# Kernel tuning notes

Hardware: AMD Instinct MI355X
Metric: run time of the kernel (lower is better)

Reference implementation:

```python
import jax, jax.numpy as jnp
import numpy as np


def setup_inputs() -> dict:
    key = jax.random.key(0)
    ks = jax.random.split(key, 9)
    B, D_IN, UNITS, TOPICS, VOCAB = 64, 512, 1024, 20, 32000
    return {
        "inputs": jax.random.normal(ks[0], (B, D_IN), jnp.float32),
        "prev_state": jax.random.normal(ks[1], (B, UNITS), jnp.float32),
        "kernel": jax.random.normal(ks[2], (D_IN, UNITS), jnp.float32) * 0.02,
        "recurrent_kernel": jax.random.normal(ks[3], (UNITS, UNITS), jnp.float32) * 0.02,
        "bernoli_kernel": jax.random.normal(ks[4], (UNITS, 1), jnp.float32) * 0.02,
        "vocab_kernel": jax.random.normal(ks[5], (UNITS, VOCAB), jnp.float32) * 0.02,
        "beta": jax.random.normal(ks[6], (TOPICS, VOCAB), jnp.float32),
        "indicators": jax.random.randint(ks[7], (B,), 0, 2, jnp.int32),
        "indices": jax.random.randint(ks[8], (B,), 0, VOCAB, jnp.int32),
    }


def reference(inputs, prev_state, kernel, recurrent_kernel, bernoli_kernel,
              vocab_kernel, beta, indicators, indices):
    # h_t = x @ W_xh + h_{t-1} @ W_hh   -> [B, units]
    next_state = inputs @ kernel + prev_state @ recurrent_kernel
    # stop-word Bernoulli prob: sigmoid(softplus(h_t @ w_b))  -> [B, 1]
    bern_p = jax.nn.sigmoid(jax.nn.softplus(next_state @ bernoli_kernel))
    bern_p = bern_p[..., None]  # [B, 1, 1]
    # deterministic sampling key (reference baseline)
    samp_key = jax.random.key(42)
    bern_samples = jax.random.bernoulli(samp_key, bern_p).astype(jnp.float32)
    # logits: [B,1,V] + (1 - l_t) * beta[T,V] -> [B, T, V]
    logits = (next_state @ vocab_kernel)[:, None, :] + (1.0 - bern_samples) * beta
    word_prob_out = jax.nn.softmax(logits, axis=-1)
    return word_prob_out, next_state
```

## Files before the change

### kernel.cpp

```cpp
#include <hip/hip_runtime.h>
#include <cstdint>
#include <cstddef>

typedef unsigned int u32;
typedef unsigned short u16;

#define NB 64
#define DIN 512
#define UNITS 1024
#define TOPICS 20
#define VOCAB 32000
#define NS_OFF ((size_t)NB * TOPICS * VOCAB)
#define ESV_PART ((size_t)NB * VOCAB)

typedef __attribute__((ext_vector_type(8))) short s16x8;
typedef __attribute__((ext_vector_type(4))) float f32x4;

__device__ __forceinline__ float bf2f(u16 h) {
    union { u32 u; float f; } c; c.u = ((u32)h) << 16; return c.f;
}
__device__ __forceinline__ u16 f2bf(float f) {
    union { float f; u32 u; } c; c.f = f;
    u32 r = c.u + 0x7FFFu + ((c.u >> 16) & 1u);
    return (u16)(r >> 16);
}
template<bool F32>
__device__ __forceinline__ float ldv(const void* p, size_t i) {
    if constexpr (F32) return ((const float*)p)[i];
    else return bf2f(((const u16*)p)[i]);
}
__device__ __forceinline__ float ldr(const void* p, size_t i, bool f32) {
    return f32 ? ((const float*)p)[i] : bf2f(((const u16*)p)[i]);
}

__device__ __forceinline__ u32 threefry_bits_partitionable(u32 i) {
    const u32 ks0 = 0u, ks1 = 42u, ks2 = 0u ^ 42u ^ 0x1BD11BDAu;
    u32 x0 = 0u + ks0, x1 = i + ks1;
#define TF_R(r) { x0 += x1; x1 = (x1 << r) | (x1 >> (32 - r)); x1 ^= x0; }
    TF_R(13) TF_R(15) TF_R(26) TF_R(6)
    x0 += ks1; x1 += ks2 + 1u;
    TF_R(17) TF_R(29) TF_R(16) TF_R(24)
    x0 += ks2; x1 += ks0 + 2u;
    TF_R(13) TF_R(15) TF_R(26) TF_R(6)
    x0 += ks0; x1 += ks1 + 3u;
    TF_R(17) TF_R(29) TF_R(16) TF_R(24)
    x0 += ks1; x1 += ks2 + 4u;
    TF_R(13) TF_R(15) TF_R(26) TF_R(6)
    x0 += ks2; x1 += ks0 + 5u;
#undef TF_R
    return x0 ^ x1;
}

__global__ __launch_bounds__(256)
void k_init(const void* __restrict__ beta, int* __restrict__ flag,
            float* __restrict__ lsum, float* __restrict__ eb) {
    int tid = threadIdx.x, lane = tid & 63, w = tid >> 6;
    __shared__ int cnt_s[4];
    int cnt = 0;
    const u32* braw = (const u32*)beta;
    for (int i = tid; i < 1024; i += 256) {
        u32 x = braw[i];
        u32 e = (x >> 7) & 0xFFu;
        cnt += (e >= 110u && e <= 132u) ? 1 : 0;
    }
    for (int off = 32; off; off >>= 1) cnt += __shfl_down(cnt, off, 64);
    if (lane == 0) cnt_s[w] = cnt;
    __syncthreads();
    int total = cnt_s[0] + cnt_s[1] + cnt_s[2] + cnt_s[3];
    bool f32 = total < 512;

    size_t base = (size_t)blockIdx.x * 2000;
    for (int i = tid; i < 2000; i += 256)
        eb[base + i] = __expf(ldr(beta, base + i, f32));

    if (blockIdx.x == 0) {
        for (int i = tid; i < NB * TOPICS; i += 256) lsum[i] = 0.f;
        if (tid == 0) flag[0] = f32 ? 1 : 0;
    }
}

template<bool F32>
__device__ void state_body(const void* xin, const void* h0, const void* Wxh,
                           const void* Whh, float* ns_f32, void* dout) {
    __shared__ float lx[DIN + UNITS];
    int b = blockIdx.x >> 2;
    int u = ((blockIdx.x & 3) << 8) | threadIdx.x;
    for (int i = threadIdx.x; i < DIN; i += 256)
        lx[i] = ldv<F32>(xin, (size_t)b * DIN + i);
    for (int i = threadIdx.x; i < UNITS; i += 256)
        lx[DIN + i] = ldv<F32>(h0, (size_t)b * UNITS + i);
    __syncthreads();
    float acc = 0.f;
#pragma unroll 8
    for (int k = 0; k < DIN; ++k)   acc += lx[k]       * ldv<F32>(Wxh, (size_t)k * UNITS + u);
#pragma unroll 8
    for (int k = 0; k < UNITS; ++k) acc += lx[DIN + k] * ldv<F32>(Whh, (size_t)k * UNITS + u);
    int idx = b * UNITS + u;
    ns_f32[idx] = acc;
    if constexpr (F32) ((float*)dout)[NS_OFF + idx] = acc;
    else               ((u16*)dout)[NS_OFF + idx]   = f2bf(acc);
}
__global__ __launch_bounds__(256)
void k_state(const int* __restrict__ flag, const void* xin, const void* h0,
             const void* Wxh, const void* Whh,
             float* __restrict__ ns_f32, void* dout) {
    if (*flag) state_body<true>(xin, h0, Wxh, Whh, ns_f32, dout);
    else       state_body<false>(xin, h0, Wxh, Whh, ns_f32, dout);
}

template<bool F32>
__device__ void bern_body(const float* ns, const void* bk, float* coeff) {
    int b = blockIdx.x, lane = threadIdx.x;
    float s = 0.f;
#pragma unroll
    for (int i = 0; i < UNITS / 64; ++i) {
        int k = lane + (i << 6);
        s += ns[b * UNITS + k] * ldv<F32>(bk, k);
    }
    for (int off = 32; off; off >>= 1) s += __shfl_down(s, off, 64);
    if (lane == 0) {
        float sp = log1pf(expf(s));
        float p  = 1.f / (1.f + expf(-sp));
        u32 bits = threefry_bits_partitionable((u32)b);
        union { u32 u; float f; } c; c.u = (bits >> 9) | 0x3f800000u;
        float uni = c.f - 1.0f;
        coeff[b] = (uni < p) ? 0.f : 1.f;
    }
}
__global__ __launch_bounds__(64)
void k_bern(const int* __restrict__ flag, const float* __restrict__ ns,
            const void* bk, float* __restrict__ coeff) {
    if (*flag) bern_body<true>(ns, bk, coeff);
    else       bern_body<false>(ns, bk, coeff);
}

#define PAD 68
#define SV_BB 16384
#define SV_SMEM_BYTES 34816

__device__ void sv_mfma_body(const short* __restrict__ ns16,
                             const short* __restrict__ Wv,
                             float* __restrict__ esv4, char* smem, int pos) {
    const int tid  = threadIdx.x;
    const int lane = tid & 63;
    const int wn   = tid >> 6;
    const int g    = lane >> 4;
    const int l15  = lane & 15;

    const int vb = pos % 125, kb = pos / 125;
    const int v0 = vb * 256;
    const int kbase0 = kb * 256;

    const int w5 = tid >> 5, c31 = tid & 31;
    const short* bs0 = Wv + (size_t)(kbase0 +  0 + w5) * VOCAB + v0 + ((c31 ^ 0) << 3);
    const short* bs1 = Wv + (size_t)(kbase0 +  8 + w5) * VOCAB + v0 + ((c31 ^ 1) << 3);
    const short* bs2 = Wv + (size_t)(kbase0 + 16 + w5) * VOCAB + v0 + ((c31 ^ 2) << 3);
    const short* bs3 = Wv + (size_t)(kbase0 + 24 + w5) * VOCAB + v0 + ((c31 ^ 3) << 3);
    const short* as0 = ns16 + (size_t)(l15     ) * UNITS + kbase0 + g * 8;
    const short* as1 = ns16 + (size_t)(l15 + 16) * UNITS + kbase0 + g * 8;
    const short* as2 = ns16 + (size_t)(l15 + 32) * UNITS + kbase0 + g * 8;
    const short* as3 = ns16 + (size_t)(l15 + 48) * UNITS + kbase0 + g * 8;

    float4 bE0, bE1, bE2, bE3;
    float4 bO0, bO1, bO2, bO3;
    s16x8  aE0, aE1, aE2, aE3;
    s16x8  aO0, aO1, aO2, aO3;

    f32x4 acc[4][4];
#pragma unroll
    for (int m = 0; m < 4; ++m)
#pragma unroll
        for (int n = 0; n < 4; ++n) acc[m][n] = (f32x4){0.f, 0.f, 0.f, 0.f};

#define LOADB(T, R0, R1, R2, R3) {                                        \
    size_t ko = (size_t)(T) * 32 * VOCAB;                                 \
    R0 = *(const float4*)(bs0 + ko); R1 = *(const float4*)(bs1 + ko);     \
    R2 = *(const float4*)(bs2 + ko); R3 = *(const float4*)(bs3 + ko); }
#define LOADA(T, A0, A1, A2, A3) {                                        \
    int ko = (T) * 32;                                                    \
    A0 = *(const s16x8*)(as0 + ko); A1 = *(const s16x8*)(as1 + ko);       \
    A2 = *(const s16x8*)(as2 + ko); A3 = *(const s16x8*)(as3 + ko); }
#define WRITEB(BUF, R0, R1, R2, R3) {                                     \
    float4* d = (float4*)(smem + (BUF) * SV_BB);                          \
    d[tid] = R0; d[256 + tid] = R1; d[512 + tid] = R2; d[768 + tid] = R3; }
#define COMPUTE(BUF, A0, A1, A2, A3) {                                    \
    const short* Bs = (const short*)(smem + (BUF) * SV_BB);               \
    _Pragma("unroll")                                                     \
    for (int nf = 0; nf < 4; ++nf) {                                      \
        int col = wn * 64 + nf * 16 + l15;                                \
        int b0  = (((col >> 3) ^ g) << 3) + (col & 7);                    \
        s16x8 bf;                                                         \
        _Pragma("unroll")                                                 \
        for (int e = 0; e < 8; ++e) bf[e] = Bs[(g * 8 + e) * 256 + b0];   \
        acc[0][nf] = __builtin_amdgcn_mfma_f32_16x16x32_bf16(A0, bf, acc[0][nf], 0, 0, 0); \
        acc[1][nf] = __builtin_amdgcn_mfma_f32_16x16x32_bf16(A1, bf, acc[1][nf], 0, 0, 0); \
        acc[2][nf] = __builtin_amdgcn_mfma_f32_16x16x32_bf16(A2, bf, acc[2][nf], 0, 0, 0); \
        acc[3][nf] = __builtin_amdgcn_mfma_f32_16x16x32_bf16(A3, bf, acc[3][nf], 0, 0, 0); } }
#define VMW(N)  asm volatile("s_waitcnt vmcnt(" #N ")" ::: "memory");
#define LGK0    asm volatile("s_waitcnt lgkmcnt(0)" ::: "memory");
#define BAR     __builtin_amdgcn_s_barrier();

    LOADB(0, bE0, bE1, bE2, bE3)
    LOADA(0, aE0, aE1, aE2, aE3)
    LOADB(1, bO0, bO1, bO2, bO3)
    VMW(8)
    WRITEB(0, bE0, bE1, bE2, bE3)
    LGK0

    LOADB(2, bE0, bE1, bE2, bE3)  LOADA(1, aO0, aO1, aO2, aO3)
    BAR  VMW(8)  WRITEB(1, bO0, bO1, bO2, bO3)  LGK0
    COMPUTE(0, aE0, aE1, aE2, aE3)
    LOADB(3, bO0, bO1, bO2, bO3)  LOADA(2, aE0, aE1, aE2, aE3)
    BAR  VMW(8)  WRITEB(0, bE0, bE1, bE2, bE3)  LGK0
    COMPUTE(1, aO0, aO1, aO2, aO3)
    LOADB(4, bE0, bE1, bE2, bE3)  LOADA(3, aO0, aO1, aO2, aO3)
    BAR  VMW(8)  WRITEB(1, bO0, bO1, bO2, bO3)  LGK0
    COMPUTE(2, aE0, aE1, aE2, aE3)
    LOADB(5, bO0, bO1, bO2, bO3)  LOADA(4, aE0, aE1, aE2, aE3)
    BAR  VMW(8)  WRITEB(0, bE0, bE1, bE2, bE3)  LGK0
    COMPUTE(3, aO0, aO1, aO2, aO3)
    LOADB(6, bE0, bE1, bE2, bE3)  LOADA(5, aO0, aO1, aO2, aO3)
    BAR  VMW(8)  WRITEB(1, bO0, bO1, bO2, bO3)  LGK0
    COMPUTE(4, aE0, aE1, aE2, aE3)
    LOADB(7, bO0, bO1, bO2, bO3)  LOADA(6, aE0, aE1, aE2, aE3)
    BAR  VMW(8)  WRITEB(0, bE0, bE1, bE2, bE3)  LGK0
    COMPUTE(5, aO0, aO1, aO2, aO3)
    LOADA(7, aO0, aO1, aO2, aO3)
    BAR  VMW(4)  WRITEB(1, bO0, bO1, bO2, bO3)  LGK0
    COMPUTE(6, aE0, aE1, aE2, aE3)
    BAR  VMW(0)
    COMPUTE(7, aO0, aO1, aO2, aO3)

#undef LOADB
#undef LOADA
#undef WRITEB
#undef COMPUTE
#undef VMW
#undef LGK0
#undef BAR

    float* dst = esv4 + (size_t)kb * ESV_PART + v0;
#pragma unroll
    for (int mf = 0; mf < 4; ++mf)
#pragma unroll
        for (int nf = 0; nf < 4; ++nf) {
            int col = wn * 64 + nf * 16 + l15;
#pragma unroll
            for (int r = 0; r < 4; ++r) {
                int b = mf * 16 + (lane >> 4) * 4 + r;
                dst[(size_t)b * VOCAB + col] = acc[mf][nf][r];
            }
        }
}

__device__ void sv_f32_body(const float* __restrict__ ns, const float* __restrict__ Wv,
                            float* __restrict__ esv4, float* As, float* Bs, int pos) {
    int tid = threadIdx.x;
    int vt = tid & 7;
    int bg = tid >> 3;
    int v0 = pos * 64;
    float acc[2][8];
#pragma unroll
    for (int r = 0; r < 2; ++r)
#pragma unroll
        for (int j = 0; j < 8; ++j) acc[r][j] = 0.f;

    for (int k0 = 0; k0 < UNITS; k0 += 64) {
        __syncthreads();
        for (int e = tid; e < 1024; e += 256) {
            int row = e >> 4, c4 = e & 15;
            *(float4*)&As[row * PAD + c4 * 4] =
                *(const float4*)&ns[row * UNITS + k0 + c4 * 4];
        }
        for (int e = tid; e < 1024; e += 256) {
            int row = e >> 4, c4 = e & 15;
            *(float4*)&Bs[row * PAD + c4 * 4] =
                *(const float4*)(Wv + (size_t)(k0 + row) * VOCAB + v0 + c4 * 4);
        }
        __syncthreads();
#pragma unroll 4
        for (int u = 0; u < 64; u += 4) {
            float4 a0 = *(float4*)&As[(bg * 2 + 0) * PAD + u];
            float4 a1 = *(float4*)&As[(bg * 2 + 1) * PAD + u];
            float aa0[4] = {a0.x, a0.y, a0.z, a0.w};
            float aa1[4] = {a1.x, a1.y, a1.z, a1.w};
#pragma unroll
            for (int uu = 0; uu < 4; ++uu) {
                float4 b0 = *(float4*)&Bs[(u + uu) * PAD + vt * 8];
                float4 b1 = *(float4*)&Bs[(u + uu) * PAD + vt * 8 + 4];
                float bb[8] = {b0.x, b0.y, b0.z, b0.w, b1.x, b1.y, b1.z, b1.w};
#pragma unroll
                for (int j = 0; j < 8; ++j) {
                    acc[0][j] = fmaf(aa0[uu], bb[j], acc[0][j]);
                    acc[1][j] = fmaf(aa1[uu], bb[j], acc[1][j]);
                }
            }
        }
    }
#pragma unroll
    for (int r = 0; r < 2; ++r) {
        float4 e0 = {acc[r][0], acc[r][1], acc[r][2], acc[r][3]};
        float4 e1 = {acc[r][4], acc[r][5], acc[r][6], acc[r][7]};
        float* dst = esv4 + (size_t)(bg * 2 + r) * VOCAB + v0 + vt * 8;
        *(float4*)dst = e0;
        *(float4*)(dst + 4) = e1;
    }
}

__global__ __launch_bounds__(256, 3)
void k_sv(const int* __restrict__ flag, const float* __restrict__ ns,
          const void* Wv, const void* dout, float* __restrict__ esv4) {
    __shared__ __align__(16) char smem[SV_SMEM_BYTES];
    int lin = blockIdx.x;
    int xcd = lin & 7, idx = lin >> 3;
    int pos = (xcd < 4) ? xcd * 63 + idx : 252 + (xcd - 4) * 62 + idx;
    if (*flag) {
        float* As = (float*)smem;
        sv_f32_body(ns, (const float*)Wv, esv4, As, As + 64 * PAD, pos);
    } else {
        sv_mfma_body((const short*)dout + NS_OFF, (const short*)Wv, esv4, smem, pos);
    }
}

__global__ __launch_bounds__(256)
void k_sum(const int* __restrict__ flag, const float* __restrict__ esv4,
           const float* __restrict__ eb, const float* __restrict__ coeff,
           float* __restrict__ lsum) {
    int b = blockIdx.y, tid = threadIdx.x;
    bool f32 = (*flag != 0);
    float c = coeff[b];
    const float4* P0 = (const float4*)(esv4 + (size_t)b * VOCAB);
    const float4* P1 = (const float4*)(esv4 + ESV_PART + (size_t)b * VOCAB);
    const float4* P2 = (const float4*)(esv4 + 2 * ESV_PART + (size_t)b * VOCAB);
    const float4* P3 = (const float4*)(esv4 + 3 * ESV_PART + (size_t)b * VOCAB);
    int i0 = blockIdx.x * 256 + tid;
    __shared__ float red[4][TOPICS];
    int lane = tid & 63, w = tid >> 6;

    if (c != 0.f) {
        float acc[TOPICS];
#pragma unroll
        for (int t = 0; t < TOPICS; ++t) acc[t] = 0.f;
        for (int i = i0; i < VOCAB / 4; i += 4096) {
            float4 q = P0[i];
            if (!f32) {
                float4 a = P1[i], d = P2[i], h = P3[i];
                q.x += a.x + d.x + h.x; q.y += a.y + d.y + h.y;
                q.z += a.z + d.z + h.z; q.w += a.w + d.w + h.w;
            }
            float4 e;
            e.x = __expf(q.x); e.y = __expf(q.y);
            e.z = __expf(q.z); e.w = __expf(q.w);
#pragma unroll
            for (int t = 0; t < TOPICS; ++t) {
                float4 g = *(const float4*)(eb + (size_t)t * VOCAB + i * 4);
                acc[t] += e.x * g.x + e.y * g.y + e.z * g.z + e.w * g.w;
            }
        }
#pragma unroll
        for (int t = 0; t < TOPICS; ++t) {
            float v = acc[t];
            for (int off = 32; off; off >>= 1) v += __shfl_down(v, off, 64);
            if (lane == 0) red[w][t] = v;
        }
        __syncthreads();
        if (tid < TOPICS) {
            float s = red[0][tid] + red[1][tid] + red[2][tid] + red[3][tid];
            atomicAdd(&lsum[b * TOPICS + tid], s);
        }
    } else {
        float a = 0.f;
        for (int i = i0; i < VOCAB / 4; i += 4096) {
            float4 q = P0[i];
            if (!f32) {
                float4 x = P1[i], d = P2[i], h = P3[i];
                q.x += x.x + d.x + h.x; q.y += x.y + d.y + h.y;
                q.z += x.z + d.z + h.z; q.w += x.w + d.w + h.w;
            }
            a += __expf(q.x) + __expf(q.y) + __expf(q.z) + __expf(q.w);
        }
        for (int off = 32; off; off >>= 1) a += __shfl_down(a, off, 64);
        if (lane == 0) red[w][0] = a;
        __syncthreads();
        if (tid < TOPICS) {
            float s = red[0][0] + red[1][0] + red[2][0] + red[3][0];
            atomicAdd(&lsum[b * TOPICS + tid], s);
        }
    }
}

template<bool F32>
__device__ void write_body(const float* esv4, const float* eb, const float* coeff,
                           const float* lsum, void* dout) {
    int b = blockIdx.y, tid = threadIdx.x;
    int v0 = blockIdx.x * 2048 + tid * 8;
    if (v0 >= VOCAB) return;
    float c = coeff[b];
    const float* er = esv4 + (size_t)b * VOCAB + v0;
    float4 q0 = *(const float4*)er;
    float4 q1 = *(const float4*)(er + 4);
    if constexpr (!F32) {
#pragma unroll
        for (int p = 1; p < 4; ++p) {
            float4 a0 = *(const float4*)(er + p * ESV_PART);
            float4 a1 = *(const float4*)(er + p * ESV_PART + 4);
            q0.x += a0.x; q0.y += a0.y; q0.z += a0.z; q0.w += a0.w;
            q1.x += a1.x; q1.y += a1.y; q1.z += a1.z; q1.w += a1.w;
        }
    }
    float4 e0, e1;
    e0.x = __expf(q0.x); e0.y = __expf(q0.y); e0.z = __expf(q0.z); e0.w = __expf(q0.w);
    e1.x = __expf(q1.x); e1.y = __expf(q1.y); e1.z = __expf(q1.z); e1.w = __expf(q1.w);
#pragma unroll 4
    for (int t = 0; t < TOPICS; ++t) {
        float inv = 1.0f / lsum[b * TOPICS + t];
        float o0, o1, o2, o3, o4, o5, o6, o7;
        if (c != 0.f) {
            const float* gr = eb + (size_t)t * VOCAB + v0;
            float4 g0 = *(const float4*)gr;
            float4 g1 = *(const float4*)(gr + 4);
            o0 = e0.x * g0.x * inv; o1 = e0.y * g0.y * inv;
            o2 = e0.z * g0.z * inv; o3 = e0.w * g0.w * inv;
            o4 = e1.x * g1.x * inv; o5 = e1.y * g1.y * inv;
            o6 = e1.z * g1.z * inv; o7 = e1.w * g1.w * inv;
        } else {
            o0 = e0.x * inv; o1 = e0.y * inv; o2 = e0.z * inv; o3 = e0.w * inv;
            o4 = e1.x * inv; o5 = e1.y * inv; o6 = e1.z * inv; o7 = e1.w * inv;
        }
        size_t off = (size_t)b * TOPICS * VOCAB + (size_t)t * VOCAB + v0;
        if constexpr (F32) {
            float4 s0 = {o0, o1, o2, o3}, s1 = {o4, o5, o6, o7};
            *(float4*)((float*)dout + off) = s0;
            *(float4*)((float*)dout + off + 4) = s1;
        } else {
            uint4 st;
            st.x = (u32)f2bf(o0) | ((u32)f2bf(o1) << 16);
            st.y = (u32)f2bf(o2) | ((u32)f2bf(o3) << 16);
            st.z = (u32)f2bf(o4) | ((u32)f2bf(o5) << 16);
            st.w = (u32)f2bf(o6) | ((u32)f2bf(o7) << 16);
            *(uint4*)((u16*)dout + off) = st;
        }
    }
}
__global__ __launch_bounds__(256)
void k_write(const int* __restrict__ flag, const float* __restrict__ esv4,
             const float* __restrict__ eb, const float* __restrict__ coeff,
             const float* __restrict__ lsum, void* dout) {
    if (*flag) write_body<true>(esv4, eb, coeff, lsum, dout);
    else       write_body<false>(esv4, eb, coeff, lsum, dout);
}

extern "C" void kernel_launch(void* const* d_in, const int* in_sizes, int n_in,
                              void* d_out, int out_size, void* d_ws, size_t ws_size,
                              hipStream_t stream) {
    const void* xin  = d_in[0];
    const void* h0   = d_in[1];
    const void* Wxh  = d_in[2];
    const void* Whh  = d_in[3];
    const void* bk   = d_in[4];
    const void* Wv   = d_in[5];
    const void* beta = d_in[6];

    char* ws = (char*)d_ws;
    int*   flag   = (int*)  (ws + 0);
    float* coeff  = (float*)(ws + 256);
    float* lsum   = (float*)(ws + 1024);
    float* ns_f32 = (float*)(ws + 8192);
    float* eb     = (float*)(ws + 270336);
    float* esv4   = (float*)(ws + 2830336);

    k_init <<<320, 256, 0, stream>>>(beta, flag, lsum, eb);
    k_state<<<256, 256, 0, stream>>>(flag, xin, h0, Wxh, Whh, ns_f32, d_out);
    k_bern <<<64, 64, 0, stream>>>(flag, ns_f32, bk, coeff);
    k_sv   <<<500, 256, 0, stream>>>(flag, ns_f32, Wv, d_out, esv4);
    k_sum  <<<dim3(16, 64), 256, 0, stream>>>(flag, esv4, eb, coeff, lsum);
    k_write<<<dim3(16, 64), 256, 0, stream>>>(flag, esv4, eb, coeff, lsum, d_out);
}
```

Before: 483.7 us.

## Split state GEMM over K halves and split vocab GEMM into four K-launches

The recurrent-state GEMM is split into two K halves across twice as many blocks, and the partial sums are added in the Bernoulli kernel, which now also writes next_state to the output. The vocab GEMM tile is narrowed from 256 to 64 columns per block and issued as four separate launches, one per 256-wide K chunk, each writing its own partial-sum slab. The f32 path now also produces four partials, so the sum and write kernels always add them. The aim is more parallelism and less per-block register and shared-memory pressure, at the cost of extra launches, partial-sum traffic and less B-tile reuse per block.

```diff
diff --git a/kernel.cpp b/kernel.cpp
--- a/kernel.cpp
+++ b/kernel.cpp
@@ -81,41 +81,52 @@
 
 template<bool F32>
 __device__ void state_body(const void* xin, const void* h0, const void* Wxh,
-                           const void* Whh, float* ns_f32, void* dout) {
-    __shared__ float lx[DIN + UNITS];
-    int b = blockIdx.x >> 2;
-    int u = ((blockIdx.x & 3) << 8) | threadIdx.x;
-    for (int i = threadIdx.x; i < DIN; i += 256)
-        lx[i] = ldv<F32>(xin, (size_t)b * DIN + i);
-    for (int i = threadIdx.x; i < UNITS; i += 256)
-        lx[DIN + i] = ldv<F32>(h0, (size_t)b * UNITS + i);
+                           const void* Whh, float* ns_p) {
+    __shared__ float lx[768];
+    int bid  = blockIdx.x;
+    int b    = bid >> 3;
+    int uq   = (bid >> 1) & 3;
+    int half = bid & 1;
+    int u = (uq << 8) | threadIdx.x;
+    for (int i = threadIdx.x; i < 768; i += 256) {
+        int kk = half * 768 + i;
+        lx[i] = (kk < DIN) ? ldv<F32>(xin, (size_t)b * DIN + kk)
+                           : ldv<F32>(h0,  (size_t)b * UNITS + (kk - DIN));
+    }
     __syncthreads();
     float acc = 0.f;
+    if (half == 0) {
 #pragma unroll 8
-    for (int k = 0; k < DIN; ++k)   acc += lx[k]       * ldv<F32>(Wxh, (size_t)k * UNITS + u);
+        for (int k = 0; k < DIN; ++k) acc += lx[k] * ldv<F32>(Wxh, (size_t)k * UNITS + u);
 #pragma unroll 8
-    for (int k = 0; k < UNITS; ++k) acc += lx[DIN + k] * ldv<F32>(Whh, (size_t)k * UNITS + u);
-    int idx = b * UNITS + u;
-    ns_f32[idx] = acc;
-    if constexpr (F32) ((float*)dout)[NS_OFF + idx] = acc;
-    else               ((u16*)dout)[NS_OFF + idx]   = f2bf(acc);
+        for (int k = 0; k < 256; ++k) acc += lx[DIN + k] * ldv<F32>(Whh, (size_t)k * UNITS + u);
+    } else {
+#pragma unroll 8
+        for (int k = 0; k < 768; ++k) acc += lx[k] * ldv<F32>(Whh, (size_t)(256 + k) * UNITS + u);
+    }
+    ns_p[half * (NB * UNITS) + b * UNITS + u] = acc;
 }
 __global__ __launch_bounds__(256)
 void k_state(const int* __restrict__ flag, const void* xin, const void* h0,
-             const void* Wxh, const void* Whh,
-             float* __restrict__ ns_f32, void* dout) {
-    if (*flag) state_body<true>(xin, h0, Wxh, Whh, ns_f32, dout);
-    else       state_body<false>(xin, h0, Wxh, Whh, ns_f32, dout);
+             const void* Wxh, const void* Whh, float* __restrict__ ns_p) {
+    if (*flag) state_body<true>(xin, h0, Wxh, Whh, ns_p);
+    else       state_body<false>(xin, h0, Wxh, Whh, ns_p);
 }
 
 template<bool F32>
-__device__ void bern_body(const float* ns, const void* bk, float* coeff) {
+__device__ void bern_body(const float* ns_p, const void* bk, float* coeff,
+                          float* ns_f32, void* dout) {
     int b = blockIdx.x, lane = threadIdx.x;
     float s = 0.f;
 #pragma unroll
     for (int i = 0; i < UNITS / 64; ++i) {
         int k = lane + (i << 6);
-        s += ns[b * UNITS + k] * ldv<F32>(bk, k);
+        int idx = b * UNITS + k;
+        float v = ns_p[idx] + ns_p[NB * UNITS + idx];
+        ns_f32[idx] = v;
+        if constexpr (F32) ((float*)dout)[NS_OFF + idx] = v;
+        else               ((u16*)dout)[NS_OFF + idx]   = f2bf(v);
+        s += v * ldv<F32>(bk, k);
     }
     for (int off = 32; off; off >>= 1) s += __shfl_down(s, off, 64);
     if (lane == 0) {
@@ -128,105 +139,94 @@
     }
 }
 __global__ __launch_bounds__(64)
-void k_bern(const int* __restrict__ flag, const float* __restrict__ ns,
-            const void* bk, float* __restrict__ coeff) {
-    if (*flag) bern_body<true>(ns, bk, coeff);
-    else       bern_body<false>(ns, bk, coeff);
+void k_bern(const int* __restrict__ flag, const float* __restrict__ ns_p,
+            const void* bk, float* __restrict__ coeff,
+            float* __restrict__ ns_f32, void* dout) {
+    if (*flag) bern_body<true>(ns_p, bk, coeff, ns_f32, dout);
+    else       bern_body<false>(ns_p, bk, coeff, ns_f32, dout);
 }
 
 #define PAD 68
-#define SV_BB 16384
+#define SV_BB 4096
 #define SV_SMEM_BYTES 34816
 
 __device__ void sv_mfma_body(const short* __restrict__ ns16,
                              const short* __restrict__ Wv,
-                             float* __restrict__ esv4, char* smem, int pos) {
+                             float* __restrict__ esv4, char* smem,
+                             int pos, int kb) {
     const int tid  = threadIdx.x;
     const int lane = tid & 63;
     const int wn   = tid >> 6;
     const int g    = lane >> 4;
     const int l15  = lane & 15;
 
-    const int vb = pos % 125, kb = pos / 125;
-    const int v0 = vb * 256;
+    const int v0 = pos * 64;
     const int kbase0 = kb * 256;
 
-    const int w5 = tid >> 5, c31 = tid & 31;
-    const short* bs0 = Wv + (size_t)(kbase0 +  0 + w5) * VOCAB + v0 + ((c31 ^ 0) << 3);
-    const short* bs1 = Wv + (size_t)(kbase0 +  8 + w5) * VOCAB + v0 + ((c31 ^ 1) << 3);
-    const short* bs2 = Wv + (size_t)(kbase0 + 16 + w5) * VOCAB + v0 + ((c31 ^ 2) << 3);
-    const short* bs3 = Wv + (size_t)(kbase0 + 24 + w5) * VOCAB + v0 + ((c31 ^ 3) << 3);
+    const int bk_ = tid >> 3, bc_ = tid & 7;
+    const short* bsrc = Wv + (size_t)(kbase0 + bk_) * VOCAB + v0
+                      + ((bc_ ^ (bk_ >> 3)) << 3);
     const short* as0 = ns16 + (size_t)(l15     ) * UNITS + kbase0 + g * 8;
     const short* as1 = ns16 + (size_t)(l15 + 16) * UNITS + kbase0 + g * 8;
     const short* as2 = ns16 + (size_t)(l15 + 32) * UNITS + kbase0 + g * 8;
     const short* as3 = ns16 + (size_t)(l15 + 48) * UNITS + kbase0 + g * 8;
 
-    float4 bE0, bE1, bE2, bE3;
-    float4 bO0, bO1, bO2, bO3;
+    float4 bE, bO;
     s16x8  aE0, aE1, aE2, aE3;
     s16x8  aO0, aO1, aO2, aO3;
 
-    f32x4 acc[4][4];
-#pragma unroll
-    for (int m = 0; m < 4; ++m)
-#pragma unroll
-        for (int n = 0; n < 4; ++n) acc[m][n] = (f32x4){0.f, 0.f, 0.f, 0.f};
-
-#define LOADB(T, R0, R1, R2, R3) {                                        \
-    size_t ko = (size_t)(T) * 32 * VOCAB;                                 \
-    R0 = *(const float4*)(bs0 + ko); R1 = *(const float4*)(bs1 + ko);     \
-    R2 = *(const float4*)(bs2 + ko); R3 = *(const float4*)(bs3 + ko); }
+    f32x4 acc[4];
+#pragma unroll
+    for (int m = 0; m < 4; ++m) acc[m] = (f32x4){0.f, 0.f, 0.f, 0.f};
+
+#define LOADB(T, R)  { R = *(const float4*)(bsrc + (size_t)(T) * 32 * VOCAB); }
 #define LOADA(T, A0, A1, A2, A3) {                                        \
     int ko = (T) * 32;                                                    \
     A0 = *(const s16x8*)(as0 + ko); A1 = *(const s16x8*)(as1 + ko);       \
     A2 = *(const s16x8*)(as2 + ko); A3 = *(const s16x8*)(as3 + ko); }
-#define WRITEB(BUF, R0, R1, R2, R3) {                                     \
-    float4* d = (float4*)(smem + (BUF) * SV_BB);                          \
-    d[tid] = R0; d[256 + tid] = R1; d[512 + tid] = R2; d[768 + tid] = R3; }
+#define WRITEB(BUF, R)  { ((float4*)(smem + (BUF) * SV_BB))[tid] = R; }
 #define COMPUTE(BUF, A0, A1, A2, A3) {                                    \
     const short* Bs = (const short*)(smem + (BUF) * SV_BB);               \
+    int col = wn * 16 + l15;                                              \
+    int b0  = (((col >> 3) ^ g) << 3) + (col & 7);                        \
+    s16x8 bf;                                                             \
     _Pragma("unroll")                                                     \
-    for (int nf = 0; nf < 4; ++nf) {                                      \
-        int col = wn * 64 + nf * 16 + l15;                                \
-        int b0  = (((col >> 3) ^ g) << 3) + (col & 7);                    \
-        s16x8 bf;                                                         \
-        _Pragma("unroll")                                                 \
-        for (int e = 0; e < 8; ++e) bf[e] = Bs[(g * 8 + e) * 256 + b0];   \
-        acc[0][nf] = __builtin_amdgcn_mfma_f32_16x16x32_bf16(A0, bf, acc[0][nf], 0, 0, 0); \
-        acc[1][nf] = __builtin_amdgcn_mfma_f32_16x16x32_bf16(A1, bf, acc[1][nf], 0, 0, 0); \
-        acc[2][nf] = __builtin_amdgcn_mfma_f32_16x16x32_bf16(A2, bf, acc[2][nf], 0, 0, 0); \
-        acc[3][nf] = __builtin_amdgcn_mfma_f32_16x16x32_bf16(A3, bf, acc[3][nf], 0, 0, 0); } }
+    for (int e = 0; e < 8; ++e) bf[e] = Bs[(g * 8 + e) * 64 + b0];        \
+    acc[0] = __builtin_amdgcn_mfma_f32_16x16x32_bf16(A0, bf, acc[0], 0, 0, 0); \
+    acc[1] = __builtin_amdgcn_mfma_f32_16x16x32_bf16(A1, bf, acc[1], 0, 0, 0); \
+    acc[2] = __builtin_amdgcn_mfma_f32_16x16x32_bf16(A2, bf, acc[2], 0, 0, 0); \
+    acc[3] = __builtin_amdgcn_mfma_f32_16x16x32_bf16(A3, bf, acc[3], 0, 0, 0); }
 #define VMW(N)  asm volatile("s_waitcnt vmcnt(" #N ")" ::: "memory");
 #define LGK0    asm volatile("s_waitcnt lgkmcnt(0)" ::: "memory");
 #define BAR     __builtin_amdgcn_s_barrier();
 
-    LOADB(0, bE0, bE1, bE2, bE3)
+    LOADB(0, bE)
     LOADA(0, aE0, aE1, aE2, aE3)
-    LOADB(1, bO0, bO1, bO2, bO3)
-    VMW(8)
-    WRITEB(0, bE0, bE1, bE2, bE3)
+    LOADB(1, bO)
+    VMW(5)
+    WRITEB(0, bE)
     LGK0
 
-    LOADB(2, bE0, bE1, bE2, bE3)  LOADA(1, aO0, aO1, aO2, aO3)
-    BAR  VMW(8)  WRITEB(1, bO0, bO1, bO2, bO3)  LGK0
+    LOADB(2, bE)  LOADA(1, aO0, aO1, aO2, aO3)
+    BAR  VMW(5)  WRITEB(1, bO)  LGK0
     COMPUTE(0, aE0, aE1, aE2, aE3)
-    LOADB(3, bO0, bO1, bO2, bO3)  LOADA(2, aE0, aE1, aE2, aE3)
-    BAR  VMW(8)  WRITEB(0, bE0, bE1, bE2, bE3)  LGK0
+    LOADB(3, bO)  LOADA(2, aE0, aE1, aE2, aE3)
+    BAR  VMW(5)  WRITEB(0, bE)  LGK0
     COMPUTE(1, aO0, aO1, aO2, aO3)
-    LOADB(4, bE0, bE1, bE2, bE3)  LOADA(3, aO0, aO1, aO2, aO3)
-    BAR  VMW(8)  WRITEB(1, bO0, bO1, bO2, bO3)  LGK0
+    LOADB(4, bE)  LOADA(3, aO0, aO1, aO2, aO3)
+    BAR  VMW(5)  WRITEB(1, bO)  LGK0
     COMPUTE(2, aE0, aE1, aE2, aE3)
-    LOADB(5, bO0, bO1, bO2, bO3)  LOADA(4, aE0, aE1, aE2, aE3)
-    BAR  VMW(8)  WRITEB(0, bE0, bE1, bE2, bE3)  LGK0
+    LOADB(5, bO)  LOADA(4, aE0, aE1, aE2, aE3)
+    BAR  VMW(5)  WRITEB(0, bE)  LGK0
     COMPUTE(3, aO0, aO1, aO2, aO3)
-    LOADB(6, bE0, bE1, bE2, bE3)  LOADA(5, aO0, aO1, aO2, aO3)
-    BAR  VMW(8)  WRITEB(1, bO0, bO1, bO2, bO3)  LGK0
+    LOADB(6, bE)  LOADA(5, aO0, aO1, aO2, aO3)
+    BAR  VMW(5)  WRITEB(1, bO)  LGK0
     COMPUTE(4, aE0, aE1, aE2, aE3)
-    LOADB(7, bO0, bO1, bO2, bO3)  LOADA(6, aE0, aE1, aE2, aE3)
-    BAR  VMW(8)  WRITEB(0, bE0, bE1, bE2, bE3)  LGK0
+    LOADB(7, bO)  LOADA(6, aE0, aE1, aE2, aE3)
+    BAR  VMW(5)  WRITEB(0, bE)  LGK0
     COMPUTE(5, aO0, aO1, aO2, aO3)
     LOADA(7, aO0, aO1, aO2, aO3)
-    BAR  VMW(4)  WRITEB(1, bO0, bO1, bO2, bO3)  LGK0
+    BAR  VMW(4)  WRITEB(1, bO)  LGK0
     COMPUTE(6, aE0, aE1, aE2, aE3)
     BAR  VMW(0)
     COMPUTE(7, aO0, aO1, aO2, aO3)
@@ -240,21 +240,19 @@
 #undef BAR
 
     float* dst = esv4 + (size_t)kb * ESV_PART + v0;
+    const int col = wn * 16 + l15;
 #pragma unroll
     for (int mf = 0; mf < 4; ++mf)
 #pragma unroll
-        for (int nf = 0; nf < 4; ++nf) {
-            int col = wn * 64 + nf * 16 + l15;
-#pragma unroll
-            for (int r = 0; r < 4; ++r) {
-                int b = mf * 16 + (lane >> 4) * 4 + r;
-                dst[(size_t)b * VOCAB + col] = acc[mf][nf][r];
-            }
+        for (int r = 0; r < 4; ++r) {
+            int b = mf * 16 + (lane >> 4) * 4 + r;
+            dst[(size_t)b * VOCAB + col] = acc[mf][r];
         }
 }
 
 __device__ void sv_f32_body(const float* __restrict__ ns, const float* __restrict__ Wv,
-                            float* __restrict__ esv4, float* As, float* Bs, int pos) {
+                            float* __restrict__ esv4, float* As, float* Bs,
+                            int pos, int kb) {
     int tid = threadIdx.x;
     int vt = tid & 7;
     int bg = tid >> 3;
@@ -265,7 +263,7 @@
 #pragma unroll
         for (int j = 0; j < 8; ++j) acc[r][j] = 0.f;
 
-    for (int k0 = 0; k0 < UNITS; k0 += 64) {
+    for (int k0 = kb * 256; k0 < kb * 256 + 256; k0 += 64) {
         __syncthreads();
         for (int e = tid; e < 1024; e += 256) {
             int row = e >> 4, c4 = e & 15;
@@ -297,11 +295,12 @@
             }
         }
     }
+    float* base = esv4 + (size_t)kb * ESV_PART;
 #pragma unroll
     for (int r = 0; r < 2; ++r) {
         float4 e0 = {acc[r][0], acc[r][1], acc[r][2], acc[r][3]};
         float4 e1 = {acc[r][4], acc[r][5], acc[r][6], acc[r][7]};
-        float* dst = esv4 + (size_t)(bg * 2 + r) * VOCAB + v0 + vt * 8;
+        float* dst = base + (size_t)(bg * 2 + r) * VOCAB + v0 + vt * 8;
         *(float4*)dst = e0;
         *(float4*)(dst + 4) = e1;
     }
@@ -309,25 +308,24 @@
 
 __global__ __launch_bounds__(256, 3)
 void k_sv(const int* __restrict__ flag, const float* __restrict__ ns,
-          const void* Wv, const void* dout, float* __restrict__ esv4) {
+          const void* Wv, const void* dout, float* __restrict__ esv4, int kb) {
     __shared__ __align__(16) char smem[SV_SMEM_BYTES];
     int lin = blockIdx.x;
     int xcd = lin & 7, idx = lin >> 3;
     int pos = (xcd < 4) ? xcd * 63 + idx : 252 + (xcd - 4) * 62 + idx;
     if (*flag) {
         float* As = (float*)smem;
-        sv_f32_body(ns, (const float*)Wv, esv4, As, As + 64 * PAD, pos);
+        sv_f32_body(ns, (const float*)Wv, esv4, As, As + 64 * PAD, pos, kb);
     } else {
-        sv_mfma_body((const short*)dout + NS_OFF, (const short*)Wv, esv4, smem, pos);
+        sv_mfma_body((const short*)dout + NS_OFF, (const short*)Wv, esv4, smem,
+                     pos, kb);
     }
 }
 
 __global__ __launch_bounds__(256)
-void k_sum(const int* __restrict__ flag, const float* __restrict__ esv4,
-           const float* __restrict__ eb, const float* __restrict__ coeff,
-           float* __restrict__ lsum) {
+void k_sum(const float* __restrict__ esv4, const float* __restrict__ eb,
+           const float* __restrict__ coeff, float* __restrict__ lsum) {
     int b = blockIdx.y, tid = threadIdx.x;
-    bool f32 = (*flag != 0);
     float c = coeff[b];
     const float4* P0 = (const float4*)(esv4 + (size_t)b * VOCAB);
     const float4* P1 = (const float4*)(esv4 + ESV_PART + (size_t)b * VOCAB);
@@ -343,11 +341,9 @@
         for (int t = 0; t < TOPICS; ++t) acc[t] = 0.f;
         for (int i = i0; i < VOCAB / 4; i += 4096) {
             float4 q = P0[i];
-            if (!f32) {
-                float4 a = P1[i], d = P2[i], h = P3[i];
-                q.x += a.x + d.x + h.x; q.y += a.y + d.y + h.y;
-                q.z += a.z + d.z + h.z; q.w += a.w + d.w + h.w;
-            }
+            float4 a = P1[i], d = P2[i], h = P3[i];
+            q.x += a.x + d.x + h.x; q.y += a.y + d.y + h.y;
+            q.z += a.z + d.z + h.z; q.w += a.w + d.w + h.w;
             float4 e;
             e.x = __expf(q.x); e.y = __expf(q.y);
             e.z = __expf(q.z); e.w = __expf(q.w);
@@ -372,11 +368,9 @@
         float a = 0.f;
         for (int i = i0; i < VOCAB / 4; i += 4096) {
             float4 q = P0[i];
-            if (!f32) {
-                float4 x = P1[i], d = P2[i], h = P3[i];
-                q.x += x.x + d.x + h.x; q.y += x.y + d.y + h.y;
-                q.z += x.z + d.z + h.z; q.w += x.w + d.w + h.w;
-            }
+            float4 x = P1[i], d = P2[i], h = P3[i];
+            q.x += x.x + d.x + h.x; q.y += x.y + d.y + h.y;
+            q.z += x.z + d.z + h.z; q.w += x.w + d.w + h.w;
             a += __expf(q.x) + __expf(q.y) + __expf(q.z) + __expf(q.w);
         }
         for (int off = 32; off; off >>= 1) a += __shfl_down(a, off, 64);
@@ -399,14 +393,12 @@
     const float* er = esv4 + (size_t)b * VOCAB + v0;
     float4 q0 = *(const float4*)er;
     float4 q1 = *(const float4*)(er + 4);
-    if constexpr (!F32) {
-#pragma unroll
-        for (int p = 1; p < 4; ++p) {
-            float4 a0 = *(const float4*)(er + p * ESV_PART);
-            float4 a1 = *(const float4*)(er + p * ESV_PART + 4);
-            q0.x += a0.x; q0.y += a0.y; q0.z += a0.z; q0.w += a0.w;
-            q1.x += a1.x; q1.y += a1.y; q1.z += a1.z; q1.w += a1.w;
-        }
+#pragma unroll
+    for (int p = 1; p < 4; ++p) {
+        float4 a0 = *(const float4*)(er + p * ESV_PART);
+        float4 a1 = *(const float4*)(er + p * ESV_PART + 4);
+        q0.x += a0.x; q0.y += a0.y; q0.z += a0.z; q0.w += a0.w;
+        q1.x += a1.x; q1.y += a1.y; q1.z += a1.z; q1.w += a1.w;
     }
     float4 e0, e1;
     e0.x = __expf(q0.x); e0.y = __expf(q0.y); e0.z = __expf(q0.z); e0.w = __expf(q0.w);
@@ -468,11 +460,15 @@
     float* ns_f32 = (float*)(ws + 8192);
     float* eb     = (float*)(ws + 270336);
     float* esv4   = (float*)(ws + 2830336);
+    float* ns_p   = esv4;
 
     k_init <<<320, 256, 0, stream>>>(beta, flag, lsum, eb);
-    k_state<<<256, 256, 0, stream>>>(flag, xin, h0, Wxh, Whh, ns_f32, d_out);
-    k_bern <<<64, 64, 0, stream>>>(flag, ns_f32, bk, coeff);
-    k_sv   <<<500, 256, 0, stream>>>(flag, ns_f32, Wv, d_out, esv4);
-    k_sum  <<<dim3(16, 64), 256, 0, stream>>>(flag, esv4, eb, coeff, lsum);
+    k_state<<<512, 256, 0, stream>>>(flag, xin, h0, Wxh, Whh, ns_p);
+    k_bern <<<64, 64, 0, stream>>>(flag, ns_p, bk, coeff, ns_f32, d_out);
+    k_sv   <<<500, 256, 0, stream>>>(flag, ns_f32, Wv, d_out, esv4, 0);
+    k_sv   <<<500, 256, 0, stream>>>(flag, ns_f32, Wv, d_out, esv4, 1);
+    k_sv   <<<500, 256, 0, stream>>>(flag, ns_f32, Wv, d_out, esv4, 2);
+    k_sv   <<<500, 256, 0, stream>>>(flag, ns_f32, Wv, d_out, esv4, 3);
+    k_sum  <<<dim3(16, 64), 256, 0, stream>>>(esv4, eb, coeff, lsum);
     k_write<<<dim3(16, 64), 256, 0, stream>>>(flag, esv4, eb, coeff, lsum, d_out);
 }
```

Result: faster. 464.3 us (-4.0%).
